# Performance work log

Measured on AMD Instinct MI355X. Metric: run time of the kernel, lower is better.

## Reference

```python
import jax, jax.numpy as jnp
import numpy as np

NUM_HEADS = 12
HEAD_DIM = 64
HIDDEN = NUM_HEADS * HEAD_DIM  # 768
B, L = 4, 512

def setup_inputs() -> dict:
    key = jax.random.key(0)
    ks = jax.random.split(key, 8)
    s = 0.02
    return {
        "hidden_states": jax.random.normal(ks[0], (B, L, HIDDEN), jnp.float32),
        "relation_embedding_k": jax.random.normal(ks[1], (B, L, L, HEAD_DIM), jnp.float32),
        "relation_embedding_v": jax.random.normal(ks[2], (B, L, L, HEAD_DIM), jnp.float32),
        "Wq": jax.random.normal(ks[3], (HIDDEN, HIDDEN), jnp.float32) * s,
        "bq": jnp.zeros((HIDDEN,), jnp.float32),
        "Wk": jax.random.normal(ks[4], (HIDDEN, HIDDEN), jnp.float32) * s,
        "bk": jnp.zeros((HIDDEN,), jnp.float32),
        "Wv": jax.random.normal(ks[5], (HIDDEN, HIDDEN), jnp.float32) * s,
        "bv": jnp.zeros((HIDDEN,), jnp.float32),
    }

def _heads(x):
    # [B, L, HIDDEN] -> [B, H, L, D]
    b, l, _ = x.shape
    return x.reshape(b, l, NUM_HEADS, HEAD_DIM).transpose(0, 2, 1, 3)

def reference(hidden_states, relation_embedding_k, relation_embedding_v,
              Wq, bq, Wk, bk, Wv, bv):
    q = _heads(hidden_states @ Wq + bq)  # [B,H,L,D]
    k = _heads(hidden_states @ Wk + bk)
    v = _heads(hidden_states @ Wv + bv)

    # content scores + relation key scores (shared across heads)
    scores = jnp.einsum('bhld,bhmd->bhlm', q, k)
    scores = scores + jnp.einsum('bhld,blrd->bhlr', q, relation_embedding_k)
    scores = scores / np.sqrt(HEAD_DIM).astype(np.float32)

    probs = jax.nn.softmax(scores, axis=-1)  # [B,H,L,L]

    ctx = jnp.einsum('bhlm,bhmd->bhld', probs, v)
    ctx = ctx + jnp.einsum('bhlr,brld->bhld', probs, relation_embedding_v)

    # [B,H,L,D] -> [B,L,HIDDEN]
    b, h, l, d = ctx.shape
    return ctx.transpose(0, 2, 1, 3).reshape(b, l, h * d)
```

## Files before the change

### kernel.cpp

```cpp
#include <hip/hip_runtime.h>
#include <stdint.h>


typedef __attribute__((ext_vector_type(8))) short bf16x8;
typedef __attribute__((ext_vector_type(4))) float f32x4;
typedef __attribute__((ext_vector_type(4))) unsigned int u32x4;

__device__ __forceinline__ unsigned short f2bf(float f) {
  union { float f; unsigned int u; } v; v.f = f;
  unsigned int r = v.u + 0x7fffu + ((v.u >> 16) & 1u);
  return (unsigned short)(r >> 16);
}
__device__ __forceinline__ float bf2f(unsigned short s) {
  union { unsigned int u; float f; } v; v.u = ((unsigned int)s) << 16;
  return v.f;
}
__device__ __forceinline__ void lds_barrier() {
  asm volatile("s_waitcnt lgkmcnt(0)\ns_barrier" ::: "memory");
}
__device__ __forceinline__ unsigned cvtpk(float lo, float hi) {
  unsigned r;
  asm("v_cvt_pk_bf16_f32 %0, %1, %2" : "=v"(r) : "v"(lo), "v"(hi));
  return r;
}

#define GL16(dst, addr, OFF)                                                  \
  asm volatile("global_load_dwordx4 %0, %1, off offset:" #OFF                \
               : "=v"(dst) : "v"(addr))
#define WAITV(N)                                                              \
  do {                                                                        \
    asm volatile("s_waitcnt vmcnt(" #N ")" ::: "memory");                     \
    __builtin_amdgcn_sched_barrier(0);                                        \
  } while (0)

__global__ void k_cvt_hidden(const float* __restrict__ x, unsigned short* __restrict__ y) {
  int i = blockIdx.x * 256 + threadIdx.x;
  float4 v = reinterpret_cast<const float4*>(x)[i];
  ushort4 o;
  o.x = f2bf(v.x); o.y = f2bf(v.y); o.z = f2bf(v.z); o.w = f2bf(v.w);
  reinterpret_cast<ushort4*>(y)[i] = o;
}

__global__ void k_transp_w(const float* __restrict__ Wq, const float* __restrict__ Wk,
                           const float* __restrict__ Wv, unsigned short* __restrict__ wt) {
  __shared__ float t[64][65];
  const int kt = blockIdx.x, nt = blockIdx.y, wsel = blockIdx.z;
  const float* W = wsel == 0 ? Wq : (wsel == 1 ? Wk : Wv);
  const int lx = threadIdx.x & 63, ly = threadIdx.x >> 6;
  for (int i = 0; i < 64; i += 4)
    t[ly + i][lx] = W[(size_t)(kt * 64 + ly + i) * 768 + nt * 64 + lx];
  __syncthreads();
  for (int i = 0; i < 64; i += 4) {
    int r = ly + i;
    wt[((size_t)wsel * 768 + nt * 64 + r) * 768 + kt * 64 + lx] = f2bf(t[lx][r]);
  }
}

__global__ __launch_bounds__(256) void k_qkv_gemm(
    const unsigned short* __restrict__ A, const unsigned short* __restrict__ Bt,
    const float* __restrict__ bq, const float* __restrict__ bk, const float* __restrict__ bv,
    unsigned short* __restrict__ qbf, unsigned short* __restrict__ kbf,
    unsigned short* __restrict__ vbt) {
  __shared__ __align__(16) unsigned short lA[64 * 64];
  __shared__ __align__(16) unsigned short lB[64 * 64];
  const int tid = threadIdx.x, lane = tid & 63, w = tid >> 6;
  const int m0 = blockIdx.x * 64, n0 = blockIdx.y * 64;
  const int wm = (w >> 1) * 32, wn = (w & 1) * 32;
  f32x4 acc[2][2] = {};

  for (int kt = 0; kt < 12; ++kt) {
    __syncthreads();
#pragma unroll
    for (int i = 0; i < 2; ++i) {
      int e16 = i * 256 + tid;
      int row = e16 >> 3;
      int kb = (e16 & 7) * 16;
      int dst = row * 128 + (kb ^ ((row & 7) << 4));
      u32x4 va = *(const u32x4*)((const char*)A + (size_t)(m0 + row) * 1536 + kt * 128 + kb);
      *(u32x4*)((char*)lA + dst) = va;
      u32x4 vb = *(const u32x4*)((const char*)Bt + (size_t)(n0 + row) * 1536 + kt * 128 + kb);
      *(u32x4*)((char*)lB + dst) = vb;
    }
    __syncthreads();
#pragma unroll
    for (int ks = 0; ks < 2; ++ks) {
      bf16x8 fa[2], fb[2];
      const int kbyte = (ks * 32 + (lane >> 4) * 8) * 2;
#pragma unroll
      for (int mi = 0; mi < 2; ++mi) {
        int row = wm + mi * 16 + (lane & 15);
        fa[mi] = *(const bf16x8*)((const char*)lA + row * 128 + (kbyte ^ ((row & 7) << 4)));
      }
#pragma unroll
      for (int ni = 0; ni < 2; ++ni) {
        int row = wn + ni * 16 + (lane & 15);
        fb[ni] = *(const bf16x8*)((const char*)lB + row * 128 + (kbyte ^ ((row & 7) << 4)));
      }
#pragma unroll
      for (int mi = 0; mi < 2; ++mi)
#pragma unroll
        for (int ni = 0; ni < 2; ++ni)
          acc[mi][ni] = __builtin_amdgcn_mfma_f32_16x16x32_bf16(fa[mi], fb[ni], acc[mi][ni], 0, 0, 0);
    }
  }
#pragma unroll
  for (int mi = 0; mi < 2; ++mi)
#pragma unroll
    for (int ni = 0; ni < 2; ++ni) {
      int gn = n0 + wn + ni * 16 + (lane & 15);
      float bias = (gn < 768) ? bq[gn] : (gn < 1536 ? bk[gn - 768] : bv[gn - 1536]);
#pragma unroll
      for (int r = 0; r < 4; ++r) {
        int gm = m0 + wm + mi * 16 + ((lane >> 4) << 2) + r;
        float val = acc[mi][ni][r] + bias;
        int b = gm >> 9, l = gm & 511;
        int d = gn & 63;
        if (gn < 768) {
          int h = gn >> 6;
          qbf[(((size_t)(b * 12 + h)) * 512 + l) * 64 + d] = f2bf(val);
        } else if (gn < 1536) {
          int h = (gn - 768) >> 6;
          kbf[(((size_t)(b * 12 + h)) * 512 + l) * 64 + d] = f2bf(val);
        } else {
          int h = (gn - 1536) >> 6;
          vbt[(((size_t)(b * 12 + h)) * 64 + d) * 512 + l] = f2bf(val);
        }
      }
    }
}

__global__ __launch_bounds__(256) void k_scores(
    const unsigned short* __restrict__ qbf, const unsigned short* __restrict__ kbf,
    float* __restrict__ S) {
  __shared__ __align__(16) unsigned short lQ[64 * 64];
  __shared__ __align__(16) unsigned short lK[64 * 64];
  const int tid = threadIdx.x, lane = tid & 63, w = tid >> 6;
  const int mt = blockIdx.x, lt = blockIdx.y, bh = blockIdx.z;
  const int wm = (w >> 1) * 32, wn = (w & 1) * 32;
  f32x4 acc[2][2] = {};
#pragma unroll
  for (int i = 0; i < 2; ++i) {
    int e16 = i * 256 + tid;
    int row = e16 >> 3;
    int kb = (e16 & 7) * 16;
    int dst = row * 128 + (kb ^ ((row & 7) << 4));
    u32x4 vq = *(const u32x4*)((const char*)qbf + ((size_t)bh * 512 + lt * 64 + row) * 128 + kb);
    *(u32x4*)((char*)lQ + dst) = vq;
    u32x4 vk = *(const u32x4*)((const char*)kbf + ((size_t)bh * 512 + mt * 64 + row) * 128 + kb);
    *(u32x4*)((char*)lK + dst) = vk;
  }
  __syncthreads();
#pragma unroll
  for (int ks = 0; ks < 2; ++ks) {
    bf16x8 fa[2], fb[2];
    const int kbyte = (ks * 32 + (lane >> 4) * 8) * 2;
#pragma unroll
    for (int mi = 0; mi < 2; ++mi) {
      int row = wm + mi * 16 + (lane & 15);
      fa[mi] = *(const bf16x8*)((const char*)lQ + row * 128 + (kbyte ^ ((row & 7) << 4)));
    }
#pragma unroll
    for (int ni = 0; ni < 2; ++ni) {
      int row = wn + ni * 16 + (lane & 15);
      fb[ni] = *(const bf16x8*)((const char*)lK + row * 128 + (kbyte ^ ((row & 7) << 4)));
    }
#pragma unroll
    for (int mi = 0; mi < 2; ++mi)
#pragma unroll
      for (int ni = 0; ni < 2; ++ni)
        acc[mi][ni] = __builtin_amdgcn_mfma_f32_16x16x32_bf16(fa[mi], fb[ni], acc[mi][ni], 0, 0, 0);
  }
#pragma unroll
  for (int mi = 0; mi < 2; ++mi)
#pragma unroll
    for (int ni = 0; ni < 2; ++ni) {
      int gm = mt * 64 + wn + ni * 16 + (lane & 15);
#pragma unroll
      for (int r = 0; r < 4; ++r) {
        int gl = lt * 64 + wm + mi * 16 + ((lane >> 4) << 2) + r;
        S[(size_t)bh * 262144 + (size_t)gl * 512 + gm] = acc[mi][ni][r];
      }
    }
}

__global__ __launch_bounds__(256) void k_relA(
    const unsigned short* __restrict__ qbf,
    const float* __restrict__ relk,
    const float* __restrict__ S,
    unsigned short* __restrict__ pbf) {
  __shared__ __align__(16) char X[24576];
  const int tid = threadIdx.x, lane = tid & 63, w = tid >> 6;
  const int bl = blockIdx.x, b = bl >> 9, l = bl & 511;
  const int lm = lane & 15, lg = lane >> 4;
  const int hq = lm < 12 ? lm : 11;

  union { f32x4 f; bf16x8 b; } qa0, qa1;
  const char* aQ = (const char*)qbf + (((size_t)b * 12 + hq) * 512 + l) * 128 + (size_t)lg * 16;
  GL16(qa0.f, aQ, 0);
  GL16(qa1.f, aQ, 64);

  const char* aA = (const char*)relk + (size_t)bl * 131072 +
                   (size_t)(w * 128 + lm) * 256 + (size_t)lg * 32;
  f32x4 td[2][4];
#define TISSUE(t, s)                                                          \
  do {                                                                        \
    const char* p_ = aA + (size_t)(t) * 4096;                                 \
    GL16(td[s][0], p_, 0);   GL16(td[s][1], p_, 16);                          \
    GL16(td[s][2], p_, 128); GL16(td[s][3], p_, 144);                         \
  } while (0)
#define ACONSUME(t, s)                                                        \
  do {                                                                        \
    union { bf16x8 v; unsigned u[4]; } fb0, fb1;                              \
    fb0.u[0] = cvtpk(td[s][0][0], td[s][0][1]);                               \
    fb0.u[1] = cvtpk(td[s][0][2], td[s][0][3]);                               \
    fb0.u[2] = cvtpk(td[s][1][0], td[s][1][1]);                               \
    fb0.u[3] = cvtpk(td[s][1][2], td[s][1][3]);                               \
    fb1.u[0] = cvtpk(td[s][2][0], td[s][2][1]);                               \
    fb1.u[1] = cvtpk(td[s][2][2], td[s][2][3]);                               \
    fb1.u[2] = cvtpk(td[s][3][0], td[s][3][1]);                               \
    fb1.u[3] = cvtpk(td[s][3][2], td[s][3][3]);                               \
    f32x4 acc = {0.f, 0.f, 0.f, 0.f};                                         \
    acc = __builtin_amdgcn_mfma_f32_16x16x32_bf16(qa0.b, fb0.v, acc, 0, 0, 0);\
    acc = __builtin_amdgcn_mfma_f32_16x16x32_bf16(qa1.b, fb1.v, acc, 0, 0, 0);\
    if (lg < 3) {                                                             \
      const int r_ = w * 128 + (t) * 16 + lm;                                 \
      _Pragma("unroll")                                                       \
      for (int reg = 0; reg < 4; ++reg)                                       \
        *(float*)(X + (lg * 4 + reg) * 2048 + ((r_ * 4) ^ (lg << 6))) =       \
            acc[reg];                                                         \
    }                                                                         \
  } while (0)

  TISSUE(0, 0); TISSUE(1, 1);
  WAITV(4); ACONSUME(0, 0); TISSUE(2, 0);
  WAITV(4); ACONSUME(1, 1); TISSUE(3, 1);
  WAITV(4); ACONSUME(2, 0); TISSUE(4, 0);
  WAITV(4); ACONSUME(3, 1); TISSUE(5, 1);
  WAITV(4); ACONSUME(4, 0); TISSUE(6, 0);
  WAITV(4); ACONSUME(5, 1); TISSUE(7, 1);
  WAITV(4); ACONSUME(6, 0);
  WAITV(0); ACONSUME(7, 1);
#undef TISSUE
#undef ACONSUME

  lds_barrier();

#pragma unroll
  for (int hh = 0; hh < 3; ++hh) {
    const int h = w * 3 + hh;
    const int sw = ((h >> 2) & 3) << 6;
    const size_t srow = (((size_t)b * 12 + h) * 512 + l) * 512;
    const float* sp = S + srow + lane;
    float sv[8];
    float mx = -1e30f;
#pragma unroll
    for (int j = 0; j < 8; ++j) {
      const int r = j * 64 + lane;
      float s = (*(const float*)(X + h * 2048 + ((r * 4) ^ sw)) + sp[j * 64]) * 0.125f;
      sv[j] = s;
      mx = fmaxf(mx, s);
    }
#pragma unroll
    for (int off = 32; off; off >>= 1) mx = fmaxf(mx, __shfl_xor(mx, off));
    float sm = 0.f;
#pragma unroll
    for (int j = 0; j < 8; ++j) { sv[j] = __expf(sv[j] - mx); sm += sv[j]; }
#pragma unroll
    for (int off = 32; off; off >>= 1) sm += __shfl_xor(sm, off);
    const float inv = 1.f / sm;
#pragma unroll
    for (int j = 0; j < 8; ++j)
      pbf[srow + j * 64 + lane] = f2bf(sv[j] * inv);
  }
}

__global__ __launch_bounds__(256) void k_relv(
    const unsigned short* __restrict__ pbf,
    const float* __restrict__ relv,
    float* __restrict__ part) {
  __shared__ __align__(16) char PS[49152];
  const int tid = threadIdx.x, lane = tid & 63, w = tid >> 6;
  const int lg = blockIdx.x, rc = blockIdx.y, b = blockIdx.z;
  const int l0 = lg * 16, r0 = rc * 128;

  {
    const int x = tid & 15, rowb = tid >> 4;
#pragma unroll
    for (int pass = 0; pass < 12; ++pass) {
      const int ri = pass * 16 + rowb;
      const int h = ri >> 4, lr = ri & 15;
      const char* src = (const char*)pbf +
          ((((size_t)b * 12 + h) * 512 + l0 + lr) * 512 + r0) * 2 + (size_t)x * 16;
      u32x4 v = *(const u32x4*)src;
      *(u32x4*)(PS + h * 4096 + lr * 256 + ((x * 16) ^ ((lr & 3) << 4))) = v;
    }
  }
  __syncthreads();

  const int lr_w = w * 4 + (lane >> 4);
  const int l = l0 + lr_w;
  const char* rvb = (const char*)relv +
      (((size_t)b * 512 + r0) * 512 + l) * 256 + (size_t)(lane & 15) * 16;

  f32x4 vA[8], vB[8];
  f32x4 acc[12];
#pragma unroll
  for (int h = 0; h < 12; ++h) acc[h] = {0.f, 0.f, 0.f, 0.f};

#define VISSUE(o, buf)                                                        \
  do {                                                                        \
    GL16(buf[0], rvb + (size_t)((o) * 8 + 0) * 131072, 0);                    \
    GL16(buf[1], rvb + (size_t)((o) * 8 + 1) * 131072, 0);                    \
    GL16(buf[2], rvb + (size_t)((o) * 8 + 2) * 131072, 0);                    \
    GL16(buf[3], rvb + (size_t)((o) * 8 + 3) * 131072, 0);                    \
    GL16(buf[4], rvb + (size_t)((o) * 8 + 4) * 131072, 0);                    \
    GL16(buf[5], rvb + (size_t)((o) * 8 + 5) * 131072, 0);                    \
    GL16(buf[6], rvb + (size_t)((o) * 8 + 6) * 131072, 0);                    \
    GL16(buf[7], rvb + (size_t)((o) * 8 + 7) * 131072, 0);                    \
  } while (0)
#define VCONS(o, buf)                                                         \
  do {                                                                        \
    _Pragma("unroll")                                                         \
    for (int h = 0; h < 12; ++h) {                                            \
      bf16x8 p8 = *(const bf16x8*)(PS + h * 4096 + lr_w * 256 +               \
                                   (((o) * 16) ^ ((lr_w & 3) << 4)));         \
      _Pragma("unroll")                                                       \
      for (int j = 0; j < 8; ++j) {                                           \
        const float pf = bf2f((unsigned short)p8[j]);                         \
        acc[h] += pf * buf[j];                                                \
      }                                                                       \
    }                                                                         \
  } while (0)

  VISSUE(0, vA);
  VISSUE(1, vB);
  WAITV(8); VCONS(0, vA); VISSUE(2, vA);
  WAITV(8); VCONS(1, vB); VISSUE(3, vB);
  WAITV(8); VCONS(2, vA); VISSUE(4, vA);
  WAITV(8); VCONS(3, vB); VISSUE(5, vB);
  WAITV(8); VCONS(4, vA); VISSUE(6, vA);
  WAITV(8); VCONS(5, vB); VISSUE(7, vB);
  WAITV(8); VCONS(6, vA); VISSUE(8, vA);
  WAITV(8); VCONS(7, vB); VISSUE(9, vB);
  WAITV(8); VCONS(8, vA); VISSUE(10, vA);
  WAITV(8); VCONS(9, vB); VISSUE(11, vB);
  WAITV(8); VCONS(10, vA); VISSUE(12, vA);
  WAITV(8); VCONS(11, vB); VISSUE(13, vB);
  WAITV(8); VCONS(12, vA); VISSUE(14, vA);
  WAITV(8); VCONS(13, vB); VISSUE(15, vB);
  WAITV(8); VCONS(14, vA);
  WAITV(0); VCONS(15, vB);
#undef VISSUE
#undef VCONS

  float* op = part + ((size_t)rc * 2048 + (size_t)b * 512 + l) * 768 + (lane & 15) * 4;
#pragma unroll
  for (int h = 0; h < 12; ++h)
    *(f32x4*)(op + h * 64) = acc[h];
}

__global__ __launch_bounds__(256) void k_pv(
    const unsigned short* __restrict__ pbf, const unsigned short* __restrict__ vbt,
    const float* __restrict__ part, float* __restrict__ out) {
  __shared__ __align__(16) unsigned short lP[64 * 64];
  __shared__ __align__(16) unsigned short lV[64 * 64];
  const int tid = threadIdx.x, lane = tid & 63, w = tid >> 6;
  const int lt = blockIdx.x, bh = blockIdx.y;
  const int b = bh / 12, h = bh % 12;
  const int wm = (w >> 1) * 32, wn = (w & 1) * 32;
  f32x4 acc[2][2] = {};
  const char* pbase = (const char*)pbf + ((size_t)bh * 512 + lt * 64) * 1024;
  const char* vbase = (const char*)vbt + (size_t)bh * 64 * 1024;
  for (int kt = 0; kt < 8; ++kt) {
    __syncthreads();
#pragma unroll
    for (int i = 0; i < 2; ++i) {
      int e16 = i * 256 + tid;
      int row = e16 >> 3;
      int kb = (e16 & 7) * 16;
      int dst = row * 128 + (kb ^ ((row & 7) << 4));
      u32x4 vp = *(const u32x4*)(pbase + (size_t)row * 1024 + kt * 128 + kb);
      *(u32x4*)((char*)lP + dst) = vp;
      u32x4 vv = *(const u32x4*)(vbase + (size_t)row * 1024 + kt * 128 + kb);
      *(u32x4*)((char*)lV + dst) = vv;
    }
    __syncthreads();
#pragma unroll
    for (int ks = 0; ks < 2; ++ks) {
      bf16x8 fa[2], fb[2];
      const int kbyte = (ks * 32 + (lane >> 4) * 8) * 2;
#pragma unroll
      for (int mi = 0; mi < 2; ++mi) {
        int row = wm + mi * 16 + (lane & 15);
        fa[mi] = *(const bf16x8*)((const char*)lP + row * 128 + (kbyte ^ ((row & 7) << 4)));
      }
#pragma unroll
      for (int ni = 0; ni < 2; ++ni) {
        int row = wn + ni * 16 + (lane & 15);
        fb[ni] = *(const bf16x8*)((const char*)lV + row * 128 + (kbyte ^ ((row & 7) << 4)));
      }
#pragma unroll
      for (int mi = 0; mi < 2; ++mi)
#pragma unroll
        for (int ni = 0; ni < 2; ++ni)
          acc[mi][ni] = __builtin_amdgcn_mfma_f32_16x16x32_bf16(fa[mi], fb[ni], acc[mi][ni], 0, 0, 0);
    }
  }
#pragma unroll
  for (int mi = 0; mi < 2; ++mi)
#pragma unroll
    for (int ni = 0; ni < 2; ++ni) {
      int gd = wn + ni * 16 + (lane & 15);
#pragma unroll
      for (int r = 0; r < 4; ++r) {
        int gl = lt * 64 + wm + mi * 16 + ((lane >> 4) << 2) + r;
        size_t o = ((size_t)b * 512 + gl) * 768 + h * 64 + gd;
        out[o] = acc[mi][ni][r] + part[o] + part[o + 1572864] +
                 part[o + 2 * 1572864] + part[o + 3 * 1572864];
      }
    }
}

extern "C" void kernel_launch(void* const* d_in, const int* in_sizes, int n_in,
                              void* d_out, int out_size, void* d_ws, size_t ws_size,
                              hipStream_t stream) {
  (void)in_sizes; (void)n_in; (void)out_size; (void)ws_size;
  const float* hidden = (const float*)d_in[0];
  const float* relk   = (const float*)d_in[1];
  const float* relv   = (const float*)d_in[2];
  const float* Wq     = (const float*)d_in[3];
  const float* bq     = (const float*)d_in[4];
  const float* Wk     = (const float*)d_in[5];
  const float* bk     = (const float*)d_in[6];
  const float* Wv     = (const float*)d_in[7];
  const float* bv     = (const float*)d_in[8];
  float* out = (float*)d_out;
  char* ws = (char*)d_ws;

  unsigned short* hb  = (unsigned short*)(ws);
  unsigned short* wt  = (unsigned short*)(ws + 3145728);
  unsigned short* qbf = (unsigned short*)(ws + 6684672);
  unsigned short* kbf = (unsigned short*)(ws + 9830400);
  unsigned short* vbt = (unsigned short*)(ws + 12976128);
  float*          S   = (float*)(ws + 16121856);
  float*          part= (float*)(ws + 16121856);
  unsigned short* pbf = (unsigned short*)(ws + 66453504);

  k_cvt_hidden<<<1536, 256, 0, stream>>>(hidden, hb);
  k_transp_w<<<dim3(12, 12, 3), 256, 0, stream>>>(Wq, Wk, Wv, wt);
  k_qkv_gemm<<<dim3(32, 36), 256, 0, stream>>>(hb, wt, bq, bk, bv, qbf, kbf, vbt);
  k_scores<<<dim3(8, 8, 48), 256, 0, stream>>>(qbf, kbf, S);
  k_relA<<<2048, 256, 0, stream>>>(qbf, relk, S, pbf);
  k_relv<<<dim3(32, 4, 4), 256, 0, stream>>>(pbf, relv, part);
  k_pv<<<dim3(8, 48), 256, 0, stream>>>(pbf, vbt, part, out);
}
```

Measured before the change: 196.5 us.

## Store scores and relv partials in bf16, deepen relk/relv prefetch pipelines

The content-score matrix S and the relation-value partial sums are now stored and read as bf16 instead of fp32, halving those intermediate buffers' traffic. The register prefetch pipelines in k_relA and k_relv go from double to triple buffering, with updated wait counts and launch-bounds occupancy hints. The bf16 rounding of pre-softmax scores and partials lowers accuracy, and the extra buffers raise register pressure.

```diff
diff --git a/kernel.cpp b/kernel.cpp
--- a/kernel.cpp
+++ b/kernel.cpp
@@ -5,6 +5,7 @@
 typedef __attribute__((ext_vector_type(8))) short bf16x8;
 typedef __attribute__((ext_vector_type(4))) float f32x4;
 typedef __attribute__((ext_vector_type(4))) unsigned int u32x4;
+typedef __attribute__((ext_vector_type(2))) unsigned int u32x2;
 
 __device__ __forceinline__ unsigned short f2bf(float f) {
   union { float f; unsigned int u; } v; v.f = f;
@@ -131,7 +132,7 @@
 
 __global__ __launch_bounds__(256) void k_scores(
     const unsigned short* __restrict__ qbf, const unsigned short* __restrict__ kbf,
-    float* __restrict__ S) {
+    unsigned short* __restrict__ Sb) {
   __shared__ __align__(16) unsigned short lQ[64 * 64];
   __shared__ __align__(16) unsigned short lK[64 * 64];
   const int tid = threadIdx.x, lane = tid & 63, w = tid >> 6;
@@ -178,15 +179,15 @@
 #pragma unroll
       for (int r = 0; r < 4; ++r) {
         int gl = lt * 64 + wm + mi * 16 + ((lane >> 4) << 2) + r;
-        S[(size_t)bh * 262144 + (size_t)gl * 512 + gm] = acc[mi][ni][r];
-      }
-    }
-}
-
-__global__ __launch_bounds__(256) void k_relA(
+        Sb[(size_t)bh * 262144 + (size_t)gl * 512 + gm] = f2bf(acc[mi][ni][r]);
+      }
+    }
+}
+
+__global__ __launch_bounds__(256, 4) void k_relA(
     const unsigned short* __restrict__ qbf,
     const float* __restrict__ relk,
-    const float* __restrict__ S,
+    const unsigned short* __restrict__ Sb,
     unsigned short* __restrict__ pbf) {
   __shared__ __align__(16) char X[24576];
   const int tid = threadIdx.x, lane = tid & 63, w = tid >> 6;
@@ -201,7 +202,7 @@
 
   const char* aA = (const char*)relk + (size_t)bl * 131072 +
                    (size_t)(w * 128 + lm) * 256 + (size_t)lg * 32;
-  f32x4 td[2][4];
+  f32x4 td[3][4];
 #define TISSUE(t, s)                                                          \
   do {                                                                        \
     const char* p_ = aA + (size_t)(t) * 4096;                                 \
@@ -231,13 +232,13 @@
     }                                                                         \
   } while (0)
 
-  TISSUE(0, 0); TISSUE(1, 1);
-  WAITV(4); ACONSUME(0, 0); TISSUE(2, 0);
-  WAITV(4); ACONSUME(1, 1); TISSUE(3, 1);
-  WAITV(4); ACONSUME(2, 0); TISSUE(4, 0);
-  WAITV(4); ACONSUME(3, 1); TISSUE(5, 1);
-  WAITV(4); ACONSUME(4, 0); TISSUE(6, 0);
-  WAITV(4); ACONSUME(5, 1); TISSUE(7, 1);
+  TISSUE(0, 0); TISSUE(1, 1); TISSUE(2, 2);
+  WAITV(8); ACONSUME(0, 0); TISSUE(3, 0);
+  WAITV(8); ACONSUME(1, 1); TISSUE(4, 1);
+  WAITV(8); ACONSUME(2, 2); TISSUE(5, 2);
+  WAITV(8); ACONSUME(3, 0); TISSUE(6, 0);
+  WAITV(8); ACONSUME(4, 1); TISSUE(7, 1);
+  WAITV(8); ACONSUME(5, 2);
   WAITV(4); ACONSUME(6, 0);
   WAITV(0); ACONSUME(7, 1);
 #undef TISSUE
@@ -250,13 +251,13 @@
     const int h = w * 3 + hh;
     const int sw = ((h >> 2) & 3) << 6;
     const size_t srow = (((size_t)b * 12 + h) * 512 + l) * 512;
-    const float* sp = S + srow + lane;
+    const unsigned short* sp = Sb + srow + lane;
     float sv[8];
     float mx = -1e30f;
 #pragma unroll
     for (int j = 0; j < 8; ++j) {
       const int r = j * 64 + lane;
-      float s = (*(const float*)(X + h * 2048 + ((r * 4) ^ sw)) + sp[j * 64]) * 0.125f;
+      float s = (*(const float*)(X + h * 2048 + ((r * 4) ^ sw)) + bf2f(sp[j * 64])) * 0.125f;
       sv[j] = s;
       mx = fmaxf(mx, s);
     }
@@ -274,10 +275,10 @@
   }
 }
 
-__global__ __launch_bounds__(256) void k_relv(
+__global__ __launch_bounds__(256, 2) void k_relv(
     const unsigned short* __restrict__ pbf,
     const float* __restrict__ relv,
-    float* __restrict__ part) {
+    unsigned short* __restrict__ part) {
   __shared__ __align__(16) char PS[49152];
   const int tid = threadIdx.x, lane = tid & 63, w = tid >> 6;
   const int lg = blockIdx.x, rc = blockIdx.y, b = blockIdx.z;
@@ -302,7 +303,7 @@
   const char* rvb = (const char*)relv +
       (((size_t)b * 512 + r0) * 512 + l) * 256 + (size_t)(lane & 15) * 16;
 
-  f32x4 vA[8], vB[8];
+  f32x4 vA[8], vB[8], vC[8];
   f32x4 acc[12];
 #pragma unroll
   for (int h = 0; h < 12; ++h) acc[h] = {0.f, 0.f, 0.f, 0.f};
@@ -334,34 +335,39 @@
 
   VISSUE(0, vA);
   VISSUE(1, vB);
-  WAITV(8); VCONS(0, vA); VISSUE(2, vA);
-  WAITV(8); VCONS(1, vB); VISSUE(3, vB);
-  WAITV(8); VCONS(2, vA); VISSUE(4, vA);
-  WAITV(8); VCONS(3, vB); VISSUE(5, vB);
-  WAITV(8); VCONS(4, vA); VISSUE(6, vA);
-  WAITV(8); VCONS(5, vB); VISSUE(7, vB);
-  WAITV(8); VCONS(6, vA); VISSUE(8, vA);
-  WAITV(8); VCONS(7, vB); VISSUE(9, vB);
-  WAITV(8); VCONS(8, vA); VISSUE(10, vA);
-  WAITV(8); VCONS(9, vB); VISSUE(11, vB);
-  WAITV(8); VCONS(10, vA); VISSUE(12, vA);
-  WAITV(8); VCONS(11, vB); VISSUE(13, vB);
-  WAITV(8); VCONS(12, vA); VISSUE(14, vA);
-  WAITV(8); VCONS(13, vB); VISSUE(15, vB);
-  WAITV(8); VCONS(14, vA);
-  WAITV(0); VCONS(15, vB);
+  VISSUE(2, vC);
+  WAITV(16); VCONS(0, vA);  VISSUE(3, vA);
+  WAITV(16); VCONS(1, vB);  VISSUE(4, vB);
+  WAITV(16); VCONS(2, vC);  VISSUE(5, vC);
+  WAITV(16); VCONS(3, vA);  VISSUE(6, vA);
+  WAITV(16); VCONS(4, vB);  VISSUE(7, vB);
+  WAITV(16); VCONS(5, vC);  VISSUE(8, vC);
+  WAITV(16); VCONS(6, vA);  VISSUE(9, vA);
+  WAITV(16); VCONS(7, vB);  VISSUE(10, vB);
+  WAITV(16); VCONS(8, vC);  VISSUE(11, vC);
+  WAITV(16); VCONS(9, vA);  VISSUE(12, vA);
+  WAITV(16); VCONS(10, vB); VISSUE(13, vB);
+  WAITV(16); VCONS(11, vC); VISSUE(14, vC);
+  WAITV(16); VCONS(12, vA); VISSUE(15, vA);
+  WAITV(16); VCONS(13, vB);
+  WAITV(8);  VCONS(14, vC);
+  WAITV(0);  VCONS(15, vA);
 #undef VISSUE
 #undef VCONS
 
-  float* op = part + ((size_t)rc * 2048 + (size_t)b * 512 + l) * 768 + (lane & 15) * 4;
-#pragma unroll
-  for (int h = 0; h < 12; ++h)
-    *(f32x4*)(op + h * 64) = acc[h];
+  unsigned short* op = part + ((size_t)rc * 2048 + (size_t)b * 512 + l) * 768 + (lane & 15) * 4;
+#pragma unroll
+  for (int h = 0; h < 12; ++h) {
+    u32x2 pk;
+    pk.x = cvtpk(acc[h][0], acc[h][1]);
+    pk.y = cvtpk(acc[h][2], acc[h][3]);
+    *(u32x2*)(op + h * 64) = pk;
+  }
 }
 
 __global__ __launch_bounds__(256) void k_pv(
     const unsigned short* __restrict__ pbf, const unsigned short* __restrict__ vbt,
-    const float* __restrict__ part, float* __restrict__ out) {
+    const unsigned short* __restrict__ part, float* __restrict__ out) {
   __shared__ __align__(16) unsigned short lP[64 * 64];
   __shared__ __align__(16) unsigned short lV[64 * 64];
   const int tid = threadIdx.x, lane = tid & 63, w = tid >> 6;
@@ -415,8 +421,8 @@
       for (int r = 0; r < 4; ++r) {
         int gl = lt * 64 + wm + mi * 16 + ((lane >> 4) << 2) + r;
         size_t o = ((size_t)b * 512 + gl) * 768 + h * 64 + gd;
-        out[o] = acc[mi][ni][r] + part[o] + part[o + 1572864] +
-                 part[o + 2 * 1572864] + part[o + 3 * 1572864];
+        out[o] = acc[mi][ni][r] + bf2f(part[o]) + bf2f(part[o + 1572864]) +
+                 bf2f(part[o + 3145728]) + bf2f(part[o + 4718592]);
       }
     }
 }
@@ -442,15 +448,15 @@
   unsigned short* qbf = (unsigned short*)(ws + 6684672);
   unsigned short* kbf = (unsigned short*)(ws + 9830400);
   unsigned short* vbt = (unsigned short*)(ws + 12976128);
-  float*          S   = (float*)(ws + 16121856);
-  float*          part= (float*)(ws + 16121856);
+  unsigned short* Sb  = (unsigned short*)(ws + 16121856);
+  unsigned short* part= (unsigned short*)(ws + 16121856);
   unsigned short* pbf = (unsigned short*)(ws + 66453504);
 
   k_cvt_hidden<<<1536, 256, 0, stream>>>(hidden, hb);
   k_transp_w<<<dim3(12, 12, 3), 256, 0, stream>>>(Wq, Wk, Wv, wt);
   k_qkv_gemm<<<dim3(32, 36), 256, 0, stream>>>(hb, wt, bq, bk, bv, qbf, kbf, vbt);
-  k_scores<<<dim3(8, 8, 48), 256, 0, stream>>>(qbf, kbf, S);
-  k_relA<<<2048, 256, 0, stream>>>(qbf, relk, S, pbf);
+  k_scores<<<dim3(8, 8, 48), 256, 0, stream>>>(qbf, kbf, Sb);
+  k_relA<<<2048, 256, 0, stream>>>(qbf, relk, Sb, pbf);
   k_relv<<<dim3(32, 4, 4), 256, 0, stream>>>(pbf, relv, part);
   k_pv<<<dim3(8, 48), 256, 0, stream>>>(pbf, vbt, part, out);
 }
```

Result: faster. 186.4 us (-5.1%).
